# Performance work log

Hardware: AMD Instinct MI355X
Metric: run time of the kernel (lower is better)

## Reference

```python
import jax, jax.numpy as jnp
import numpy as np

NUM_HEADS = 8
QKV_DIM = 32
DIM = 256
MULTI_Q = QKV_DIM * NUM_HEADS  # 256
BN_EPS = 1e-5


def conv1x1_bn(x, W, gamma, beta, mean, var):
    # 1x1 conv (no bias) followed by BatchNorm2d in eval mode.
    y = jnp.einsum('bchw,oc->bohw', x, W)
    inv = gamma / jnp.sqrt(var + BN_EPS)
    return y * inv[None, :, None, None] + (beta - mean * inv)[None, :, None, None]


def setup_inputs() -> dict:
    key = jax.random.key(0)
    ks = jax.random.split(key, 16)
    B, C, H, W = 16, DIM, 64, 64
    inp = {
        'input_': jax.random.normal(ks[0], (B, C, H, W), jnp.float32),
        'key_v_input_reduction': jax.random.normal(ks[1], (B, C, 32, 32), jnp.float32),
        # to_q: Conv2d_BN(dim -> multi_q_dim)
        'Wq': jax.random.normal(ks[2], (MULTI_Q, DIM), jnp.float32) * 0.05,
        'gq': jnp.ones((MULTI_Q,), jnp.float32),
        'bq': jnp.zeros((MULTI_Q,), jnp.float32),
        'mq': jax.random.normal(ks[3], (MULTI_Q,), jnp.float32) * 0.1,
        'vq': jax.random.uniform(ks[4], (MULTI_Q,), jnp.float32, 0.5, 1.5),
        # to_kv: Conv2d_BN(dim -> qkv_dim) (one_kv_head=True, share_kv=True)
        'Wkv': jax.random.normal(ks[5], (QKV_DIM, DIM), jnp.float32) * 0.05,
        'gkv': jnp.ones((QKV_DIM,), jnp.float32),
        'bkv': jnp.zeros((QKV_DIM,), jnp.float32),
        'mkv': jax.random.normal(ks[6], (QKV_DIM,), jnp.float32) * 0.1,
        'vkv': jax.random.uniform(ks[7], (QKV_DIM,), jnp.float32, 0.5, 1.5),
        # proj: activation -> Conv2d_BN(multi_q_dim -> dim)
        'Wp': jax.random.normal(ks[8], (DIM, MULTI_Q), jnp.float32) * 0.05,
        'gp': jnp.ones((DIM,), jnp.float32),
        'bp': jnp.zeros((DIM,), jnp.float32),
        'mp': jax.random.normal(ks[9], (DIM,), jnp.float32) * 0.1,
        'vp': jax.random.uniform(ks[10], (DIM,), jnp.float32, 0.5, 1.5),
    }
    return inp


def reference(input_, key_v_input_reduction, Wq, gq, bq, mq, vq,
              Wkv, gkv, bkv, mkv, vkv, Wp, gp, bp, mp, vp):
    B, C, H, W = input_.shape
    HW = H * W
    # Q projection -> (B, nh, d, HW)
    queries = conv1x1_bn(input_, Wq, gq, bq, mq, vq).reshape(B, NUM_HEADS, QKV_DIM, HW)
    # shared K=V projection, single kv head -> (B, 1, d, HW)
    kv = conv1x1_bn(input_, Wkv, gkv, bkv, mkv, vkv).reshape(B, 1, QKV_DIM, HW)
    key = jax.nn.softmax(kv, axis=3)       # softmax over spatial positions
    query = jax.nn.softmax(queries, axis=2)  # softmax over channel dim
    value = kv
    # context = key @ value^T : (B,1,d,d)
    context = jnp.einsum('bhdn,bhen->bhde', key, value)
    # permute(0,1,3,2) then broadcast over heads, attended = context^T @ query
    ctx_t = jnp.swapaxes(context, -1, -2)   # (B,1,d,d)
    attended = jnp.einsum('bhde,bken->bkdn'.replace('h', 'o'), ctx_t[:, 0][:, None], query) if False else jnp.matmul(ctx_t, query)  # (B,nh,d,HW) via broadcast
    attended = attended.reshape(B, MULTI_Q, H, W)
    # proj: ReLU then Conv2d_BN
    out = conv1x1_bn(jax.nn.relu(attended), Wp, gp, bp, mp, vp)
    return out
```

## Files before the change

kernel.cpp:

```cpp
#include <hip/hip_runtime.h>
#include <hip/hip_bf16.h>
#include <cstdint>

typedef _Float16 f16;
typedef _Float16 f16x4 __attribute__((ext_vector_type(4)));
typedef _Float16 f16x8 __attribute__((ext_vector_type(8)));
typedef float f32x4 __attribute__((ext_vector_type(4)));

#define MFMA16(a, b, c) __builtin_amdgcn_mfma_f32_16x16x32_f16((a), (b), (c), 0, 0, 0)

constexpr int BATCH = 16;
constexpr int C     = 256;
constexpr int HW    = 4096;
constexpr int DH    = 32;
constexpr float EPS = 1e-5f;

constexpr size_t OFF_PF = 0;
constexpr size_t SZ_PF  = (size_t)BATCH * HW * C * 2;
constexpr size_t OFF_KV = OFF_PF + SZ_PF;
constexpr size_t SZ_KV  = (size_t)BATCH * DH * HW * 4;
constexpr size_t OFF_W1 = OFF_KV + SZ_KV;
constexpr size_t OFF_B1 = OFF_W1 + 147456;
constexpr size_t OFF_WP = OFF_B1 + 2048;
constexpr size_t SZ_WP  = (size_t)C * C * 2;
constexpr size_t OFF_BP = OFF_WP + SZ_WP;
constexpr size_t OFF_U  = OFF_BP + 1024;
constexpr size_t OFF_PM = OFF_U + 65536;
constexpr size_t OFF_PS = OFF_PM + 131072;

__device__ __forceinline__ f16x8 ld8(const f16* p) {
  f16x4 lo = *(const f16x4*)p;
  f16x4 hi = *(const f16x4*)(p + 4);
  return __builtin_shufflevector(lo, hi, 0, 1, 2, 3, 4, 5, 6, 7);
}

__global__ __launch_bounds__(256) void k0_prep(
    const float* __restrict__ Wq,  const float* __restrict__ gq,  const float* __restrict__ bq,
    const float* __restrict__ mq,  const float* __restrict__ vq,
    const float* __restrict__ Wkv, const float* __restrict__ gkv, const float* __restrict__ bkv,
    const float* __restrict__ mkv, const float* __restrict__ vkv,
    const float* __restrict__ Wp,  const float* __restrict__ gp,  const float* __restrict__ bp,
    const float* __restrict__ mp,  const float* __restrict__ vp,
    f16* __restrict__ WqF, float* __restrict__ b1, f16* __restrict__ WpF,
    float* __restrict__ bp2, f16* __restrict__ WkvF, float* __restrict__ U) {
  int id = blockIdx.x * 256 + threadIdx.x;
  if (id < 65536) {
    int j = id & 7, lane = (id >> 3) & 63, ot = (id >> 9) & 15, kc = id >> 13;
    int o = ot * 16 + (lane & 15), c = kc * 32 + ((lane >> 4) << 3) + j;
    float inv = gq[o] * rsqrtf(vq[o] + EPS);
    WqF[id] = (f16)(Wq[o * 256 + c] * inv);
  } else if (id < 131072) {
    int id2 = id - 65536;
    int j = id2 & 7, lane = (id2 >> 3) & 63, ot = (id2 >> 9) & 15, kc = id2 >> 13;
    int o = ot * 16 + (lane & 15), c = kc * 32 + ((lane >> 4) << 3) + j;
    float inv = gp[o] * rsqrtf(vp[o] + EPS);
    WpF[id2] = (f16)(Wp[o * 256 + c] * inv);
  } else if (id < 139264) {
    int id2 = id - 131072;
    int j = id2 & 7, lane = (id2 >> 3) & 63, ot = (id2 >> 9) & 1, kc = id2 >> 10;
    int o = ot * 16 + (lane & 15), c = kc * 32 + ((lane >> 4) << 3) + j;
    float inv = gkv[o] * rsqrtf(vkv[o] + EPS);
    WkvF[id2] = (f16)(Wkv[o * 256 + c] * inv);
  } else if (id < 139552) {
    int r = id - 139264;
    if (r < 256) { float inv = gq[r] * rsqrtf(vq[r] + EPS);   b1[r] = bq[r] - mq[r] * inv; }
    else { int e = r - 256; float inv = gkv[e] * rsqrtf(vkv[e] + EPS); b1[r] = bkv[e] - mkv[e] * inv; }
  } else if (id < 139808) {
    int o = id - 139552;
    float inv = gp[o] * rsqrtf(vp[o] + EPS);
    bp2[o] = bp[o] - mp[o] * inv;
  } else if (id < 139808 + 16384) {
    U[id - 139808] = 0.f;
  }
}

__global__ __launch_bounds__(256, 4) void p0_trans_kv(
    const float* __restrict__ X, const f16* __restrict__ WqF, const f16* __restrict__ WkvF,
    const float* __restrict__ bq1, const float* __restrict__ bkv1,
    f16* __restrict__ PF, float* __restrict__ kvo,
    float* __restrict__ pmax, float* __restrict__ psum) {
  __shared__ alignas(16) f16 xt[64 * 260];
  f16* pa = xt;
  float* kvb = (float*)xt;
  const int t = threadIdx.x, b = blockIdx.y, n0 = blockIdx.x * 64;
  const int lane = t & 63, w = t >> 6, l15 = lane & 15, quad = lane >> 4;
  const int wn = w & 1, wm = w >> 1;
  const float* Xb = X + (size_t)b * C * HW;

  {
    int n4 = (t & 15) * 4, c4 = (t >> 4) * 4;
#pragma unroll
    for (int ci = 0; ci < 4; ++ci) {
      int c0 = ci * 64 + c4;
      const float* xp = Xb + (size_t)c0 * HW + n0 + n4;
      float4 v0 = *(const float4*)&xp[0];
      float4 v1 = *(const float4*)&xp[HW];
      float4 v2 = *(const float4*)&xp[2 * HW];
      float4 v3 = *(const float4*)&xp[3 * HW];
      f16x4 w0 = {(f16)v0.x, (f16)v1.x, (f16)v2.x, (f16)v3.x};
      f16x4 w1 = {(f16)v0.y, (f16)v1.y, (f16)v2.y, (f16)v3.y};
      f16x4 w2 = {(f16)v0.z, (f16)v1.z, (f16)v2.z, (f16)v3.z};
      f16x4 w3 = {(f16)v0.w, (f16)v1.w, (f16)v2.w, (f16)v3.w};
      *(f16x4*)&xt[(n4 + 0) * 260 + c0] = w0;
      *(f16x4*)&xt[(n4 + 1) * 260 + c0] = w1;
      *(f16x4*)&xt[(n4 + 2) * 260 + c0] = w2;
      *(f16x4*)&xt[(n4 + 3) * 260 + c0] = w3;
    }
  }
  __syncthreads();

  f32x4 acc1[2][8];
  f32x4 acckv[2];
#pragma unroll
  for (int nf = 0; nf < 8; ++nf) {
    float bv = bq1[wn * 128 + nf * 16 + l15];
#pragma unroll
    for (int mf = 0; mf < 2; ++mf)
#pragma unroll
      for (int r = 0; r < 4; ++r) acc1[mf][nf][r] = bv;
  }
  {
    float bv = bkv1[wn * 16 + l15];
#pragma unroll
    for (int r = 0; r < 4; ++r) { acckv[0][r] = bv; acckv[1][r] = bv; }
  }
#pragma unroll 1
  for (int kc = 0; kc < 8; ++kc) {
    f16x8 a0 = ld8(&xt[(wm * 32 + l15) * 260 + kc * 32 + quad * 8]);
    f16x8 a1 = ld8(&xt[(wm * 32 + 16 + l15) * 260 + kc * 32 + quad * 8]);
    f16x8 bkvf = *(const f16x8*)&WkvF[((size_t)(kc * 2 + wn) * 64 + lane) * 8];
    acckv[0] = MFMA16(a0, bkvf, acckv[0]);
    acckv[1] = MFMA16(a1, bkvf, acckv[1]);
#pragma unroll
    for (int nf = 0; nf < 8; ++nf) {
      f16x8 bf = *(const f16x8*)&WqF[((size_t)(kc * 16 + wn * 8 + nf) * 64 + lane) * 8];
      acc1[0][nf] = MFMA16(a0, bf, acc1[0][nf]);
      acc1[1][nf] = MFMA16(a1, bf, acc1[1][nf]);
    }
  }

#pragma unroll
  for (int mf = 0; mf < 2; ++mf)
#pragma unroll
    for (int h = 0; h < 4; ++h) {
      f32x4 v0 = acc1[mf][h * 2], v1 = acc1[mf][h * 2 + 1];
      f32x4 mx;
#pragma unroll
      for (int r = 0; r < 4; ++r) mx[r] = fmaxf(v0[r], v1[r]);
#pragma unroll
      for (int off = 1; off <= 8; off <<= 1)
#pragma unroll
        for (int r = 0; r < 4; ++r) mx[r] = fmaxf(mx[r], __shfl_xor(mx[r], off));
      f32x4 s4;
#pragma unroll
      for (int r = 0; r < 4; ++r) {
        v0[r] = __expf(v0[r] - mx[r]); v1[r] = __expf(v1[r] - mx[r]);
        s4[r] = v0[r] + v1[r];
      }
#pragma unroll
      for (int off = 1; off <= 8; off <<= 1)
#pragma unroll
        for (int r = 0; r < 4; ++r) s4[r] += __shfl_xor(s4[r], off);
#pragma unroll
      for (int r = 0; r < 4; ++r) {
        float si = 1.f / s4[r];
        v0[r] *= si; v1[r] *= si;
      }
      acc1[mf][h * 2] = v0; acc1[mf][h * 2 + 1] = v1;
    }
  __syncthreads();

#pragma unroll
  for (int mf = 0; mf < 2; ++mf)
#pragma unroll
    for (int nf = 0; nf < 8; ++nf)
#pragma unroll
      for (int r = 0; r < 4; ++r) {
        int n = wm * 32 + mf * 16 + quad * 4 + r;
        int o = wn * 128 + nf * 16 + l15;
        pa[n * 260 + o] = (f16)acc1[mf][nf][r];
      }
  __syncthreads();

  {
    f16* PFt = PF + ((size_t)b * 64 + blockIdx.x) * 16384;
#pragma unroll
    for (int i = 0; i < 8; ++i) {
      int u = t + i * 256;
      int lu = u & 63, ntu = (u >> 6) & 3, hu = u >> 8;
      f16x8 v = ld8(&pa[(ntu * 16 + (lu & 15)) * 260 + hu * 32 + ((lu >> 4) << 3)]);
      *(f16x8*)&PFt[(size_t)u * 8] = v;
    }
  }
  __syncthreads();

#pragma unroll
  for (int r = 0; r < 4; ++r) {
    kvb[(wn * 16 + l15) * 68 + wm * 32 + quad * 4 + r]      = acckv[0][r];
    kvb[(wn * 16 + l15) * 68 + wm * 32 + 16 + quad * 4 + r] = acckv[1][r];
  }
  __syncthreads();

#pragma unroll
  for (int i = 0; i < 2; ++i) {
    int u = t + i * 256, d = u >> 4, seg = u & 15;
    float4 v = *(const float4*)&kvb[d * 68 + seg * 4];
    *(float4*)&kvo[((size_t)b * DH + d) * HW + n0 + seg * 4] = v;
  }
  {
    int d = t >> 3, j = t & 7;
    float vals[8];
#pragma unroll
    for (int q = 0; q < 8; ++q) vals[q] = kvb[d * 68 + j * 8 + q];
    float m = vals[0];
#pragma unroll
    for (int q = 1; q < 8; ++q) m = fmaxf(m, vals[q]);
#pragma unroll
    for (int off = 1; off <= 4; off <<= 1) m = fmaxf(m, __shfl_xor(m, off));
    float s = 0.f;
#pragma unroll
    for (int q = 0; q < 8; ++q) s += __expf(vals[q] - m);
#pragma unroll
    for (int off = 1; off <= 4; off <<= 1) s += __shfl_xor(s, off);
    if (j == 0) {
      pmax[((size_t)b * DH + d) * 64 + blockIdx.x] = m;
      psum[((size_t)b * DH + d) * 64 + blockIdx.x] = s;
    }
  }
}

__global__ __launch_bounds__(256, 4) void k3_ctx(
    const float* __restrict__ kv, const float* __restrict__ pmax,
    const float* __restrict__ psum, float* __restrict__ U) {
  __shared__ float cacc[32 * 33];
  __shared__ float Ms[32], SiS[32];
  const int t = threadIdx.x, b = blockIdx.y;
  const int lane = t & 63, w = t >> 6, l15 = lane & 15, quad = lane >> 4;
  for (int i = t; i < 32 * 33; i += 256) cacc[i] = 0.f;

  {
    int i = t >> 3, j = t & 7;
    const float* pm = pmax + ((size_t)b * DH + i) * 64 + j * 8;
    const float* ps = psum + ((size_t)b * DH + i) * 64 + j * 8;
    float mv[8], sv[8];
#pragma unroll
    for (int q = 0; q < 8; ++q) { mv[q] = pm[q]; sv[q] = ps[q]; }
    float M = mv[0];
#pragma unroll
    for (int q = 1; q < 8; ++q) M = fmaxf(M, mv[q]);
#pragma unroll
    for (int off = 1; off <= 4; off <<= 1) M = fmaxf(M, __shfl_xor(M, off));
    float S = 0.f;
#pragma unroll
    for (int q = 0; q < 8; ++q) S += sv[q] * __expf(mv[q] - M);
#pragma unroll
    for (int off = 1; off <= 4; off <<= 1) S += __shfl_xor(S, off);
    if (j == 0) { Ms[i] = M; SiS[i] = 1.f / S; }
  }
  __syncthreads();

  const float* kvb = kv + (size_t)b * DH * HW;
  float M0 = Ms[l15],      Si0 = SiS[l15];
  float M1 = Ms[16 + l15], Si1 = SiS[16 + l15];
  f32x4 acc[2][2] = {};
#pragma unroll
  for (int s = 0; s < 2; ++s) {
    int nb = blockIdx.x * 256 + w * 64 + s * 32 + quad * 8;
    const float* p0 = &kvb[(size_t)l15 * HW + nb];
    const float* p1 = &kvb[(size_t)(16 + l15) * HW + nb];
    float lo[8], hi[8];
    *(float4*)&lo[0] = *(const float4*)&p0[0]; *(float4*)&lo[4] = *(const float4*)&p0[4];
    *(float4*)&hi[0] = *(const float4*)&p1[0]; *(float4*)&hi[4] = *(const float4*)&p1[4];
    f16x8 A0, A1, B0, B1;
#pragma unroll
    for (int j = 0; j < 8; ++j) {
      A0[j] = (f16)lo[j]; A1[j] = (f16)hi[j];
      B0[j] = (f16)(__expf(lo[j] - M0) * Si0);
      B1[j] = (f16)(__expf(hi[j] - M1) * Si1);
    }
    acc[0][0] = MFMA16(A0, B0, acc[0][0]);
    acc[1][0] = MFMA16(A1, B0, acc[1][0]);
    acc[0][1] = MFMA16(A0, B1, acc[0][1]);
    acc[1][1] = MFMA16(A1, B1, acc[1][1]);
  }
#pragma unroll
  for (int a = 0; a < 2; ++a)
#pragma unroll
    for (int e2 = 0; e2 < 2; ++e2)
#pragma unroll
      for (int r = 0; r < 4; ++r)
        atomicAdd(&cacc[(a * 16 + quad * 4 + r) * 33 + e2 * 16 + l15], acc[a][e2][r]);
  __syncthreads();
  for (int i = t; i < 1024; i += 256)
    atomicAdd(&U[b * 1024 + (i >> 5) * 32 + (i & 31)], cacc[(i >> 5) * 33 + (i & 31)]);
}

__global__ __launch_bounds__(256, 4) void kb_mega(
    const f16* __restrict__ PF, const float* __restrict__ U,
    const f16* __restrict__ WpF, const float* __restrict__ bp1,
    float* __restrict__ out) {
  __shared__ alignas(16) f16 pa[64 * 260];
  __shared__ alignas(16) f16 ctxs[32 * 36];
  const int t = threadIdx.x, b = blockIdx.y, n0 = blockIdx.x * 64;
  const int lane = t & 63, w = t >> 6, l15 = lane & 15, quad = lane >> 4;
  const int wn = w & 1, wm = w >> 1;

  f16x8 bfp[2][4];
  {
    const f16* PFt = PF + ((size_t)b * 64 + blockIdx.x) * 16384;
#pragma unroll
    for (int hh = 0; hh < 2; ++hh)
#pragma unroll
      for (int nt = 0; nt < 4; ++nt)
        bfp[hh][nt] = *(const f16x8*)&PFt[(((size_t)(w * 2 + hh) * 4 + nt) * 64 + lane) * 8];
  }
  {
    const float4 u4 = *(const float4*)&U[b * 1024 + t * 4];
    int d = t >> 3, e4 = (t & 7) * 4;
    f16x4 pk = {(f16)u4.x, (f16)u4.y, (f16)u4.z, (f16)u4.w};
    *(f16x4*)&ctxs[d * 36 + e4] = pk;
  }
  __syncthreads();

  f32x4 datt[2][2][4] = {};
#pragma unroll
  for (int hh = 0; hh < 2; ++hh)
#pragma unroll
    for (int mt = 0; mt < 2; ++mt) {
      f16x8 af = ld8(&ctxs[(mt * 16 + l15) * 36 + quad * 8]);
      __builtin_amdgcn_s_setprio(1);
#pragma unroll
      for (int nt = 0; nt < 4; ++nt)
        datt[hh][mt][nt] = MFMA16(af, bfp[hh][nt], datt[hh][mt][nt]);
      __builtin_amdgcn_s_setprio(0);
    }
#pragma unroll
  for (int hh = 0; hh < 2; ++hh) {
    int h = w * 2 + hh;
#pragma unroll
    for (int mt = 0; mt < 2; ++mt)
#pragma unroll
      for (int nt = 0; nt < 4; ++nt)
#pragma unroll
        for (int r = 0; r < 4; ++r) {
          int n = nt * 16 + l15;
          int cc = h * 32 + mt * 16 + quad * 4 + r;
          pa[n * 260 + cc] = (f16)fmaxf(datt[hh][mt][nt][r], 0.f);
        }
  }
  __syncthreads();

  f32x4 acc2[8][2];
#pragma unroll
  for (int mf = 0; mf < 8; ++mf)
#pragma unroll
    for (int r = 0; r < 4; ++r) {
      float bv = bp1[wm * 128 + mf * 16 + quad * 4 + r];
      acc2[mf][0][r] = bv; acc2[mf][1][r] = bv;
    }
#pragma unroll 1
  for (int kc = 0; kc < 8; ++kc) {
    f16x8 bf0 = ld8(&pa[(wn * 32 + l15) * 260 + kc * 32 + quad * 8]);
    f16x8 bf1 = ld8(&pa[(wn * 32 + 16 + l15) * 260 + kc * 32 + quad * 8]);
    __builtin_amdgcn_s_setprio(1);
#pragma unroll
    for (int mf = 0; mf < 8; ++mf) {
      f16x8 af = *(const f16x8*)&WpF[((size_t)(kc * 16 + wm * 8 + mf) * 64 + lane) * 8];
      acc2[mf][0] = MFMA16(af, bf0, acc2[mf][0]);
      acc2[mf][1] = MFMA16(af, bf1, acc2[mf][1]);
    }
    __builtin_amdgcn_s_setprio(0);
  }
#pragma unroll
  for (int mf = 0; mf < 8; ++mf)
#pragma unroll
    for (int nf = 0; nf < 2; ++nf) {
      int n = n0 + wn * 32 + nf * 16 + l15;
#pragma unroll
      for (int r = 0; r < 4; ++r) {
        int o = wm * 128 + mf * 16 + quad * 4 + r;
        out[((size_t)b * C + o) * HW + n] = acc2[mf][nf][r];
      }
    }
}

extern "C" void kernel_launch(void* const* d_in, const int* in_sizes, int n_in,
                              void* d_out, int out_size, void* d_ws, size_t ws_size,
                              hipStream_t stream) {
  (void)in_sizes; (void)n_in; (void)out_size; (void)ws_size;
  const float* input = (const float*)d_in[0];
  const float* Wq  = (const float*)d_in[2];
  const float* gq  = (const float*)d_in[3];
  const float* bq  = (const float*)d_in[4];
  const float* mq  = (const float*)d_in[5];
  const float* vq  = (const float*)d_in[6];
  const float* Wkv = (const float*)d_in[7];
  const float* gkv = (const float*)d_in[8];
  const float* bkv = (const float*)d_in[9];
  const float* mkv = (const float*)d_in[10];
  const float* vkv = (const float*)d_in[11];
  const float* Wp  = (const float*)d_in[12];
  const float* gp  = (const float*)d_in[13];
  const float* bp  = (const float*)d_in[14];
  const float* mp  = (const float*)d_in[15];
  const float* vp  = (const float*)d_in[16];

  char* ws = (char*)d_ws;
  f16*   PFw = (f16*)(ws + OFF_PF);
  float* kvw = (float*)(ws + OFF_KV);
  f16*   WqF = (f16*)(ws + OFF_W1);
  f16*   WkvF= (f16*)(ws + OFF_W1 + 131072);
  float* b1  = (float*)(ws + OFF_B1);
  f16*   WpF = (f16*)(ws + OFF_WP);
  float* bp2 = (float*)(ws + OFF_BP);
  float* U   = (float*)(ws + OFF_U);
  float* pm  = (float*)(ws + OFF_PM);
  float* ps  = (float*)(ws + OFF_PS);
  float* out = (float*)d_out;

  const float* bq1  = b1;
  const float* bkv1 = b1 + 256;

  k0_prep<<<611, 256, 0, stream>>>(Wq, gq, bq, mq, vq, Wkv, gkv, bkv, mkv, vkv,
                                   Wp, gp, bp, mp, vp, WqF, b1, WpF, bp2, WkvF, U);
  p0_trans_kv<<<dim3(64, 16), 256, 0, stream>>>(input, WqF, WkvF, bq1, bkv1,
                                                PFw, kvw, pm, ps);
  k3_ctx<<<dim3(16, 16), 256, 0, stream>>>(kvw, pm, ps, U);
  kb_mega<<<dim3(64, 16), 256, 0, stream>>>(PFw, U, WpF, bp2, out);
}
```

Baseline: 205.3 us.

## Fuse context accumulation into projection kernel and prefetch weight fragments

The separate context kernel and the fp32 kv buffer round-trip are removed. Each projection block now computes its partial key-value context with MFMA and atomically adds it, along with per-channel exp sums, to global accumulators. The final kernel divides by these sums when loading the context. Max subtraction in the spatial softmax is dropped, which risks overflow for large activations. Weight fragments are also prefetched one K-step ahead in both GEMM loops, and occupancy hints are lowered to 3 to make room for the extra registers.

Result: faster. 195.7 us (-4.7%).

```diff
diff --git a/kernel.cpp b/kernel.cpp
--- a/kernel.cpp
+++ b/kernel.cpp
@@ -17,16 +17,13 @@
 
 constexpr size_t OFF_PF = 0;
 constexpr size_t SZ_PF  = (size_t)BATCH * HW * C * 2;
-constexpr size_t OFF_KV = OFF_PF + SZ_PF;
-constexpr size_t SZ_KV  = (size_t)BATCH * DH * HW * 4;
-constexpr size_t OFF_W1 = OFF_KV + SZ_KV;
+constexpr size_t OFF_W1 = OFF_PF + SZ_PF;
 constexpr size_t OFF_B1 = OFF_W1 + 147456;
 constexpr size_t OFF_WP = OFF_B1 + 2048;
 constexpr size_t SZ_WP  = (size_t)C * C * 2;
 constexpr size_t OFF_BP = OFF_WP + SZ_WP;
 constexpr size_t OFF_U  = OFF_BP + 1024;
-constexpr size_t OFF_PM = OFF_U + 65536;
-constexpr size_t OFF_PS = OFF_PM + 131072;
+constexpr size_t OFF_S  = OFF_U + 65536;
 
 __device__ __forceinline__ f16x8 ld8(const f16* p) {
   f16x4 lo = *(const f16x4*)p;
@@ -42,7 +39,8 @@
     const float* __restrict__ Wp,  const float* __restrict__ gp,  const float* __restrict__ bp,
     const float* __restrict__ mp,  const float* __restrict__ vp,
     f16* __restrict__ WqF, float* __restrict__ b1, f16* __restrict__ WpF,
-    float* __restrict__ bp2, f16* __restrict__ WkvF, float* __restrict__ U) {
+    float* __restrict__ bp2, f16* __restrict__ WkvF, float* __restrict__ U,
+    float* __restrict__ S) {
   int id = blockIdx.x * 256 + threadIdx.x;
   if (id < 65536) {
     int j = id & 7, lane = (id >> 3) & 63, ot = (id >> 9) & 15, kc = id >> 13;
@@ -69,19 +67,20 @@
     int o = id - 139552;
     float inv = gp[o] * rsqrtf(vp[o] + EPS);
     bp2[o] = bp[o] - mp[o] * inv;
-  } else if (id < 139808 + 16384) {
+  } else if (id < 156192) {
     U[id - 139808] = 0.f;
+  } else if (id < 156704) {
+    S[id - 156192] = 0.f;
   }
 }
 
-__global__ __launch_bounds__(256, 4) void p0_trans_kv(
+__global__ __launch_bounds__(256, 3) void p0_trans_kv(
     const float* __restrict__ X, const f16* __restrict__ WqF, const f16* __restrict__ WkvF,
     const float* __restrict__ bq1, const float* __restrict__ bkv1,
-    f16* __restrict__ PF, float* __restrict__ kvo,
-    float* __restrict__ pmax, float* __restrict__ psum) {
+    f16* __restrict__ PF, float* __restrict__ U, float* __restrict__ S) {
   __shared__ alignas(16) f16 xt[64 * 260];
+  __shared__ alignas(16) float kvb[32 * 68];
   f16* pa = xt;
-  float* kvb = (float*)xt;
   const int t = threadIdx.x, b = blockIdx.y, n0 = blockIdx.x * 64;
   const int lane = t & 63, w = t >> 6, l15 = lane & 15, quad = lane >> 4;
   const int wn = w & 1, wm = w >> 1;
@@ -124,18 +123,45 @@
 #pragma unroll
     for (int r = 0; r < 4; ++r) { acckv[0][r] = bv; acckv[1][r] = bv; }
   }
+  {
+    const f16* wqb = WqF + ((size_t)(wn * 8) * 64 + lane) * 8;
+    const f16* wkb = WkvF + ((size_t)wn * 64 + lane) * 8;
+    f16x8 a0 = ld8(&xt[(wm * 32 + l15) * 260 + quad * 8]);
+    f16x8 a1 = ld8(&xt[(wm * 32 + 16 + l15) * 260 + quad * 8]);
+    f16x8 vw0[4], vw1[4], vkv;
+#pragma unroll
+    for (int nf = 0; nf < 4; ++nf) vw0[nf] = *(const f16x8*)&wqb[nf * 512];
+    vkv = *(const f16x8*)&wkb[0];
 #pragma unroll 1
-  for (int kc = 0; kc < 8; ++kc) {
-    f16x8 a0 = ld8(&xt[(wm * 32 + l15) * 260 + kc * 32 + quad * 8]);
-    f16x8 a1 = ld8(&xt[(wm * 32 + 16 + l15) * 260 + kc * 32 + quad * 8]);
-    f16x8 bkvf = *(const f16x8*)&WkvF[((size_t)(kc * 2 + wn) * 64 + lane) * 8];
-    acckv[0] = MFMA16(a0, bkvf, acckv[0]);
-    acckv[1] = MFMA16(a1, bkvf, acckv[1]);
-#pragma unroll
-    for (int nf = 0; nf < 8; ++nf) {
-      f16x8 bf = *(const f16x8*)&WqF[((size_t)(kc * 16 + wn * 8 + nf) * 64 + lane) * 8];
-      acc1[0][nf] = MFMA16(a0, bf, acc1[0][nf]);
-      acc1[1][nf] = MFMA16(a1, bf, acc1[1][nf]);
+    for (int kc = 0; kc < 8; ++kc) {
+#pragma unroll
+      for (int nf = 0; nf < 4; ++nf) vw1[nf] = *(const f16x8*)&wqb[(size_t)kc * 8192 + (4 + nf) * 512];
+      f16x8 nkv;
+      if (kc < 7) nkv = *(const f16x8*)&wkb[(size_t)(kc + 1) * 1024];
+      __builtin_amdgcn_s_setprio(1);
+      acckv[0] = MFMA16(a0, vkv, acckv[0]);
+      acckv[1] = MFMA16(a1, vkv, acckv[1]);
+#pragma unroll
+      for (int nf = 0; nf < 4; ++nf) {
+        acc1[0][nf] = MFMA16(a0, vw0[nf], acc1[0][nf]);
+        acc1[1][nf] = MFMA16(a1, vw0[nf], acc1[1][nf]);
+      }
+      __builtin_amdgcn_s_setprio(0);
+      f16x8 na0, na1;
+      if (kc < 7) {
+        na0 = ld8(&xt[(wm * 32 + l15) * 260 + (kc + 1) * 32 + quad * 8]);
+        na1 = ld8(&xt[(wm * 32 + 16 + l15) * 260 + (kc + 1) * 32 + quad * 8]);
+#pragma unroll
+        for (int nf = 0; nf < 4; ++nf) vw0[nf] = *(const f16x8*)&wqb[(size_t)(kc + 1) * 8192 + nf * 512];
+      }
+      __builtin_amdgcn_s_setprio(1);
+#pragma unroll
+      for (int nf = 0; nf < 4; ++nf) {
+        acc1[0][4 + nf] = MFMA16(a0, vw1[nf], acc1[0][4 + nf]);
+        acc1[1][4 + nf] = MFMA16(a1, vw1[nf], acc1[1][4 + nf]);
+      }
+      __builtin_amdgcn_s_setprio(0);
+      a0 = na0; a1 = na1; vkv = nkv;
     }
   }
 
@@ -180,6 +206,11 @@
         int o = wn * 128 + nf * 16 + l15;
         pa[n * 260 + o] = (f16)acc1[mf][nf][r];
       }
+#pragma unroll
+  for (int r = 0; r < 4; ++r) {
+    kvb[(wn * 16 + l15) * 68 + wm * 32 + quad * 4 + r]      = acckv[0][r];
+    kvb[(wn * 16 + l15) * 68 + wm * 32 + 16 + quad * 4 + r] = acckv[1][r];
+  }
   __syncthreads();
 
   {
@@ -192,111 +223,40 @@
       *(f16x8*)&PFt[(size_t)u * 8] = v;
     }
   }
-  __syncthreads();
-
-#pragma unroll
-  for (int r = 0; r < 4; ++r) {
-    kvb[(wn * 16 + l15) * 68 + wm * 32 + quad * 4 + r]      = acckv[0][r];
-    kvb[(wn * 16 + l15) * 68 + wm * 32 + 16 + quad * 4 + r] = acckv[1][r];
-  }
-  __syncthreads();
-
-#pragma unroll
-  for (int i = 0; i < 2; ++i) {
-    int u = t + i * 256, d = u >> 4, seg = u & 15;
-    float4 v = *(const float4*)&kvb[d * 68 + seg * 4];
-    *(float4*)&kvo[((size_t)b * DH + d) * HW + n0 + seg * 4] = v;
-  }
+
+  {
+    int dh = wn, eh = wm;
+    f32x4 cx = {0.f, 0.f, 0.f, 0.f};
+#pragma unroll
+    for (int ks = 0; ks < 2; ++ks) {
+      f16x8 A, B;
+#pragma unroll
+      for (int j = 0; j < 8; ++j) {
+        float av = kvb[(dh * 16 + l15) * 68 + ks * 32 + quad * 8 + j];
+        float bv = kvb[(eh * 16 + l15) * 68 + ks * 32 + quad * 8 + j];
+        A[j] = (f16)av;
+        B[j] = (f16)__expf(bv);
+      }
+      cx = MFMA16(A, B, cx);
+    }
+#pragma unroll
+    for (int r = 0; r < 4; ++r)
+      atomicAdd(&U[b * 1024 + (dh * 16 + quad * 4 + r) * 32 + eh * 16 + l15], cx[r]);
+  }
+
   {
     int d = t >> 3, j = t & 7;
-    float vals[8];
-#pragma unroll
-    for (int q = 0; q < 8; ++q) vals[q] = kvb[d * 68 + j * 8 + q];
-    float m = vals[0];
-#pragma unroll
-    for (int q = 1; q < 8; ++q) m = fmaxf(m, vals[q]);
-#pragma unroll
-    for (int off = 1; off <= 4; off <<= 1) m = fmaxf(m, __shfl_xor(m, off));
     float s = 0.f;
 #pragma unroll
-    for (int q = 0; q < 8; ++q) s += __expf(vals[q] - m);
+    for (int q = 0; q < 8; ++q) s += __expf(kvb[d * 68 + j * 8 + q]);
 #pragma unroll
     for (int off = 1; off <= 4; off <<= 1) s += __shfl_xor(s, off);
-    if (j == 0) {
-      pmax[((size_t)b * DH + d) * 64 + blockIdx.x] = m;
-      psum[((size_t)b * DH + d) * 64 + blockIdx.x] = s;
-    }
+    if (j == 0) atomicAdd(&S[b * 32 + d], s);
   }
 }
 
-__global__ __launch_bounds__(256, 4) void k3_ctx(
-    const float* __restrict__ kv, const float* __restrict__ pmax,
-    const float* __restrict__ psum, float* __restrict__ U) {
-  __shared__ float cacc[32 * 33];
-  __shared__ float Ms[32], SiS[32];
-  const int t = threadIdx.x, b = blockIdx.y;
-  const int lane = t & 63, w = t >> 6, l15 = lane & 15, quad = lane >> 4;
-  for (int i = t; i < 32 * 33; i += 256) cacc[i] = 0.f;
-
-  {
-    int i = t >> 3, j = t & 7;
-    const float* pm = pmax + ((size_t)b * DH + i) * 64 + j * 8;
-    const float* ps = psum + ((size_t)b * DH + i) * 64 + j * 8;
-    float mv[8], sv[8];
-#pragma unroll
-    for (int q = 0; q < 8; ++q) { mv[q] = pm[q]; sv[q] = ps[q]; }
-    float M = mv[0];
-#pragma unroll
-    for (int q = 1; q < 8; ++q) M = fmaxf(M, mv[q]);
-#pragma unroll
-    for (int off = 1; off <= 4; off <<= 1) M = fmaxf(M, __shfl_xor(M, off));
-    float S = 0.f;
-#pragma unroll
-    for (int q = 0; q < 8; ++q) S += sv[q] * __expf(mv[q] - M);
-#pragma unroll
-    for (int off = 1; off <= 4; off <<= 1) S += __shfl_xor(S, off);
-    if (j == 0) { Ms[i] = M; SiS[i] = 1.f / S; }
-  }
-  __syncthreads();
-
-  const float* kvb = kv + (size_t)b * DH * HW;
-  float M0 = Ms[l15],      Si0 = SiS[l15];
-  float M1 = Ms[16 + l15], Si1 = SiS[16 + l15];
-  f32x4 acc[2][2] = {};
-#pragma unroll
-  for (int s = 0; s < 2; ++s) {
-    int nb = blockIdx.x * 256 + w * 64 + s * 32 + quad * 8;
-    const float* p0 = &kvb[(size_t)l15 * HW + nb];
-    const float* p1 = &kvb[(size_t)(16 + l15) * HW + nb];
-    float lo[8], hi[8];
-    *(float4*)&lo[0] = *(const float4*)&p0[0]; *(float4*)&lo[4] = *(const float4*)&p0[4];
-    *(float4*)&hi[0] = *(const float4*)&p1[0]; *(float4*)&hi[4] = *(const float4*)&p1[4];
-    f16x8 A0, A1, B0, B1;
-#pragma unroll
-    for (int j = 0; j < 8; ++j) {
-      A0[j] = (f16)lo[j]; A1[j] = (f16)hi[j];
-      B0[j] = (f16)(__expf(lo[j] - M0) * Si0);
-      B1[j] = (f16)(__expf(hi[j] - M1) * Si1);
-    }
-    acc[0][0] = MFMA16(A0, B0, acc[0][0]);
-    acc[1][0] = MFMA16(A1, B0, acc[1][0]);
-    acc[0][1] = MFMA16(A0, B1, acc[0][1]);
-    acc[1][1] = MFMA16(A1, B1, acc[1][1]);
-  }
-#pragma unroll
-  for (int a = 0; a < 2; ++a)
-#pragma unroll
-    for (int e2 = 0; e2 < 2; ++e2)
-#pragma unroll
-      for (int r = 0; r < 4; ++r)
-        atomicAdd(&cacc[(a * 16 + quad * 4 + r) * 33 + e2 * 16 + l15], acc[a][e2][r]);
-  __syncthreads();
-  for (int i = t; i < 1024; i += 256)
-    atomicAdd(&U[b * 1024 + (i >> 5) * 32 + (i & 31)], cacc[(i >> 5) * 33 + (i & 31)]);
-}
-
-__global__ __launch_bounds__(256, 4) void kb_mega(
-    const f16* __restrict__ PF, const float* __restrict__ U,
+__global__ __launch_bounds__(256, 3) void kb_mega(
+    const f16* __restrict__ PF, const float* __restrict__ U, const float* __restrict__ S,
     const f16* __restrict__ WpF, const float* __restrict__ bp1,
     float* __restrict__ out) {
   __shared__ alignas(16) f16 pa[64 * 260];
@@ -317,7 +277,9 @@
   {
     const float4 u4 = *(const float4*)&U[b * 1024 + t * 4];
     int d = t >> 3, e4 = (t & 7) * 4;
-    f16x4 pk = {(f16)u4.x, (f16)u4.y, (f16)u4.z, (f16)u4.w};
+    const float4 s4 = *(const float4*)&S[b * 32 + e4];
+    f16x4 pk = {(f16)(u4.x / s4.x), (f16)(u4.y / s4.y),
+                (f16)(u4.z / s4.z), (f16)(u4.w / s4.w)};
     *(f16x4*)&ctxs[d * 36 + e4] = pk;
   }
   __syncthreads();
@@ -358,18 +320,31 @@
       float bv = bp1[wm * 128 + mf * 16 + quad * 4 + r];
       acc2[mf][0][r] = bv; acc2[mf][1][r] = bv;
     }
+  {
+    const f16* wb = WpF + ((size_t)(wm * 8) * 64 + lane) * 8;
+    f16x8 vw[8];
+#pragma unroll
+    for (int mf = 0; mf < 8; ++mf) vw[mf] = *(const f16x8*)&wb[mf * 512];
 #pragma unroll 1
-  for (int kc = 0; kc < 8; ++kc) {
-    f16x8 bf0 = ld8(&pa[(wn * 32 + l15) * 260 + kc * 32 + quad * 8]);
-    f16x8 bf1 = ld8(&pa[(wn * 32 + 16 + l15) * 260 + kc * 32 + quad * 8]);
-    __builtin_amdgcn_s_setprio(1);
-#pragma unroll
-    for (int mf = 0; mf < 8; ++mf) {
-      f16x8 af = *(const f16x8*)&WpF[((size_t)(kc * 16 + wm * 8 + mf) * 64 + lane) * 8];
-      acc2[mf][0] = MFMA16(af, bf0, acc2[mf][0]);
-      acc2[mf][1] = MFMA16(af, bf1, acc2[mf][1]);
-    }
-    __builtin_amdgcn_s_setprio(0);
+    for (int kc = 0; kc < 8; ++kc) {
+      f16x8 nw[8];
+      if (kc < 7) {
+        const f16* wb2 = wb + (size_t)(kc + 1) * 8192;
+#pragma unroll
+        for (int mf = 0; mf < 8; ++mf) nw[mf] = *(const f16x8*)&wb2[mf * 512];
+      }
+      f16x8 bf0 = ld8(&pa[(wn * 32 + l15) * 260 + kc * 32 + quad * 8]);
+      f16x8 bf1 = ld8(&pa[(wn * 32 + 16 + l15) * 260 + kc * 32 + quad * 8]);
+      __builtin_amdgcn_s_setprio(1);
+#pragma unroll
+      for (int mf = 0; mf < 8; ++mf) {
+        acc2[mf][0] = MFMA16(vw[mf], bf0, acc2[mf][0]);
+        acc2[mf][1] = MFMA16(vw[mf], bf1, acc2[mf][1]);
+      }
+      __builtin_amdgcn_s_setprio(0);
+#pragma unroll
+      for (int mf = 0; mf < 8; ++mf) vw[mf] = nw[mf];
+    }
   }
 #pragma unroll
   for (int mf = 0; mf < 8; ++mf)
@@ -407,24 +382,21 @@
 
   char* ws = (char*)d_ws;
   f16*   PFw = (f16*)(ws + OFF_PF);
-  float* kvw = (float*)(ws + OFF_KV);
   f16*   WqF = (f16*)(ws + OFF_W1);
   f16*   WkvF= (f16*)(ws + OFF_W1 + 131072);
   float* b1  = (float*)(ws + OFF_B1);
   f16*   WpF = (f16*)(ws + OFF_WP);
   float* bp2 = (float*)(ws + OFF_BP);
   float* U   = (float*)(ws + OFF_U);
-  float* pm  = (float*)(ws + OFF_PM);
-  float* ps  = (float*)(ws + OFF_PS);
+  float* S   = (float*)(ws + OFF_S);
   float* out = (float*)d_out;
 
   const float* bq1  = b1;
   const float* bkv1 = b1 + 256;
 
-  k0_prep<<<611, 256, 0, stream>>>(Wq, gq, bq, mq, vq, Wkv, gkv, bkv, mkv, vkv,
-                                   Wp, gp, bp, mp, vp, WqF, b1, WpF, bp2, WkvF, U);
+  k0_prep<<<613, 256, 0, stream>>>(Wq, gq, bq, mq, vq, Wkv, gkv, bkv, mkv, vkv,
+                                   Wp, gp, bp, mp, vp, WqF, b1, WpF, bp2, WkvF, U, S);
   p0_trans_kv<<<dim3(64, 16), 256, 0, stream>>>(input, WqF, WkvF, bq1, bkv1,
-                                                PFw, kvw, pm, ps);
-  k3_ctx<<<dim3(16, 16), 256, 0, stream>>>(kvw, pm, ps, U);
-  kb_mega<<<dim3(64, 16), 256, 0, stream>>>(PFw, U, WpF, bp2, out);
+                                                PFw, U, S);
+  kb_mega<<<dim3(64, 16), 256, 0, stream>>>(PFw, U, S, WpF, bp2, out);
 }
```
